# Optimization experiments

Measured on AMD Instinct MI355X. Metric: run time of the kernel, lower is better.

Reference implementation:

```python
import jax, jax.numpy as jnp
import numpy as np

KS = 3          # kernel size
PAD = 1         # padding
N = KS * KS     # number of sampling taps (9)


def setup_inputs() -> dict:
    key = jax.random.key(0)
    k0, k1, k2 = jax.random.split(key, 3)
    B, Cin, Cout, H, W = 4, 64, 64, 128, 128
    x = jax.random.normal(k0, (B, Cin, H, W), jnp.float32)
    # offset conv is zero-initialized in the original; use small random weights
    # so the sampling pattern is actually irregular (post-training behavior)
    w_off = jax.random.normal(k1, (2 * N, Cin, KS, KS), jnp.float32) * 0.05
    b_off = jnp.zeros((2 * N,), jnp.float32)
    w_def = jax.random.normal(k2, (Cout, Cin, KS, KS), jnp.float32) / np.float32(np.sqrt(Cin * N))
    b_def = jnp.zeros((Cout,), jnp.float32)
    return {"x": x, "w_off": w_off, "b_off": b_off, "w_def": w_def, "b_def": b_def}


def _conv3x3(x, w, b):
    y = jax.lax.conv_general_dilated(
        x, w, window_strides=(1, 1), padding=((PAD, PAD), (PAD, PAD)),
        dimension_numbers=("NCHW", "OIHW", "NCHW"))
    return y + b[None, :, None, None]


def _deform_forward(x, w_off, b_off, w_def, b_def):
    B, C, H, W = x.shape
    Cout = w_def.shape[0]
    offset = _conv3x3(x, w_off, b_off)                 # [B, 2N, H, W]

    xp = jnp.pad(x, ((0, 0), (0, 0), (PAD, PAD), (PAD, PAD)))  # zero pad
    Hp, Wp = H + 2 * PAD, W + 2 * PAD

    # sampling positions p = p0 + pn + offset (coords in padded frame)
    r = jnp.arange(-(KS // 2), KS // 2 + 1, dtype=x.dtype)
    pn_x = jnp.repeat(r, KS)          # [-1,-1,-1, 0,0,0, 1,1,1]
    pn_y = jnp.tile(r, KS)            # [-1, 0, 1, ...]
    p0x = jnp.arange(1, H + 1, dtype=x.dtype)[None, :, None, None]  # [1,H,1,1]
    p0y = jnp.arange(1, W + 1, dtype=x.dtype)[None, None, :, None]  # [1,1,W,1]
    offx = offset[:, :N].transpose(0, 2, 3, 1)          # [B,H,W,N]
    offy = offset[:, N:].transpose(0, 2, 3, 1)
    px = p0x + pn_x[None, None, None, :] + offx          # [B,H,W,N]
    py = p0y + pn_y[None, None, None, :] + offy

    # integer corners (floor has zero grad == detach in torch ref)
    flx, fly = jnp.floor(px), jnp.floor(py)
    qlx = jnp.clip(flx, 0, Hp - 1)
    qly = jnp.clip(fly, 0, Wp - 1)
    qrx = jnp.clip(flx + 1, 0, Hp - 1)
    qry = jnp.clip(fly + 1, 0, Wp - 1)
    pxc = jnp.clip(px, 0, Hp - 1)
    pyc = jnp.clip(py, 0, Wp - 1)

    # bilinear weights (matches torch DeformConv2D formulas)
    g_lt = (1 + (qlx - pxc)) * (1 + (qly - pyc))
    g_rb = (1 - (qrx - pxc)) * (1 - (qry - pyc))
    g_lb = (1 + (qlx - pxc)) * (1 - (qry - pyc))
    g_rt = (1 - (qrx - pxc)) * (1 + (qly - pyc))

    xf = xp.reshape(B, C, Hp * Wp)

    def gather(xfb, ix, iy):
        idx = (ix * Wp + iy).astype(jnp.int32).reshape(-1)
        return xfb[:, idx].reshape(C, H, W, N)

    g4 = jax.vmap(gather)
    x_lt = g4(xf, qlx, qly)   # [B,C,H,W,N]
    x_rb = g4(xf, qrx, qry)
    x_lb = g4(xf, qlx, qry)
    x_rt = g4(xf, qrx, qly)

    x_off = (g_lt[:, None] * x_lt + g_rb[:, None] * x_rb
             + g_lb[:, None] * x_lb + g_rt[:, None] * x_rt)  # [B,C,H,W,N]

    out = jnp.einsum("bchwn,ocn->bohw", x_off, w_def.reshape(Cout, C, N))
    return out + b_def[None, :, None, None]


def reference(x, w_off, b_off, w_def, b_def):
    return _deform_forward(x, w_off, b_off, w_def, b_def)
```

## Files before the change

kernel.cpp:

```cpp
#include <hip/hip_runtime.h>

#define B_   4
#define CIN  64
#define COUT 64
#define H_   128
#define W_   128
#define NOFF 18
#define HW   (H_ * W_)
#define HP   130
#define WP   130

typedef __attribute__((ext_vector_type(8))) short bf16x8;
typedef __attribute__((ext_vector_type(4))) float f32x4;

__device__ __forceinline__ unsigned short f2bf(float f) {
    unsigned int u = __float_as_uint(f);
    return (unsigned short)((u + 0x7fffu + ((u >> 16) & 1u)) >> 16);
}

__global__ __launch_bounds__(256) void k_wt(
    const float* __restrict__ w_def, const float* __restrict__ w_off,
    unsigned short* __restrict__ wB, unsigned short* __restrict__ wBo)
{
    const int i = blockIdx.x * 256 + threadIdx.x;
    if (i < 18 * 4 * 64) {
        const int kblk = i >> 8;
        const int nblk = (i >> 6) & 3;
        const int lane = i & 63;
        const int o = nblk * 16 + (lane & 15);
        unsigned int pk[4];
#pragma unroll
        for (int d = 0; d < 4; ++d) {
            unsigned int v = 0;
#pragma unroll
            for (int e = 0; e < 2; ++e) {
                const int K = kblk * 32 + 8 * (lane >> 4) + d * 2 + e;
                const int n = K >> 6, c = K & 63;
                v |= (unsigned int)f2bf(w_def[((size_t)o * 64 + c) * 9 + n]) << (16 * e);
            }
            pk[d] = v;
        }
        *(uint4*)(wB + (size_t)i * 8) = make_uint4(pk[0], pk[1], pk[2], pk[3]);
    }
    const int j = i - 18 * 4 * 64;
    if (j >= 0 && j < 18 * 2 * 64) {
        const int kblk = j >> 7;
        const int nblk = (j >> 6) & 1;
        const int lane = j & 63;
        const int o = nblk * 16 + (lane & 15);
        unsigned int pk[4];
#pragma unroll
        for (int d = 0; d < 4; ++d) {
            unsigned int v = 0;
#pragma unroll
            for (int e = 0; e < 2; ++e) {
                const int K = kblk * 32 + 8 * (lane >> 4) + d * 2 + e;
                const int n = K >> 6, c = K & 63;
                const float wv = (o < NOFF) ? w_off[((size_t)o * 64 + c) * 9 + n] : 0.f;
                v |= (unsigned int)f2bf(wv) << (16 * e);
            }
            pk[d] = v;
        }
        *(uint4*)(wBo + (size_t)j * 8) = make_uint4(pk[0], pk[1], pk[2], pk[3]);
    }
}

__global__ __launch_bounds__(256) void k_prep(
    const float* __restrict__ x, unsigned short* __restrict__ xt,
    unsigned int* __restrict__ xt2)
{
    const int b  = blockIdx.x / HP;
    const int hp = blockIdx.x - b * HP;
    const int c  = threadIdx.x & 63;
    const int wq = threadIdx.x >> 6;
    const float* xr = x + (((size_t)b * CIN + c) * H_ + (hp - 1)) * W_;
    unsigned short* d1 = xt  + (((size_t)b * HP + hp) * WP) * 64 + c;
    unsigned int*   d2 = xt2 + (((size_t)b * HP + hp) * WP) * 64 + c;
    const bool hin = (hp >= 1 && hp <= H_);
    for (int wp = wq; wp < WP; wp += 4) {
        float v1 = 0.f, v2 = 0.f;
        if (hin) {
            if (wp >= 1 && wp <= W_)       v1 = xr[wp - 1];
            if (wp + 1 >= 1 && wp + 1 <= W_) v2 = xr[wp];
        }
        const unsigned int a1 = f2bf(v1), a2 = f2bf(v2);
        d1[(size_t)wp * 64] = (unsigned short)a1;
        d2[(size_t)wp * 64] = a1 | (a2 << 16);
    }
}

__global__ __launch_bounds__(256) void k_mega(
    const unsigned short* __restrict__ xt, const unsigned int* __restrict__ xt2,
    const unsigned short* __restrict__ wBo, const unsigned short* __restrict__ wB,
    const float* __restrict__ b_off, const float* __restrict__ b_def,
    unsigned short* __restrict__ xoff, float* __restrict__ out)
{
    __shared__ float  off_s[NOFF][64];
    __shared__ uint2  geoI[9][64];
    __shared__ float4 geoG[9][64];

    const int tid   = threadIdx.x;
    const int lane  = tid & 63;
    const int wv    = tid >> 6;
    const int row   = lane & 15;
    const int g     = lane >> 4;
    const int pxblk = blockIdx.x;
    const int b     = pxblk >> 8;
    const int h     = (pxblk >> 1) & 127;
    const int w0    = (pxblk & 1) * 64;

    {
        const unsigned short* xtb = xt + (size_t)b * (HP * WP * 64);
        const unsigned short* Bp  = wBo + (size_t)lane * 8;
        f32x4 acc0 = {0.f, 0.f, 0.f, 0.f};
        f32x4 acc1 = {0.f, 0.f, 0.f, 0.f};
#pragma unroll
        for (int kb = 0; kb < 18; ++kb) {
            const int n  = kb >> 1;
            const int hp = h + n / 3;
            const int wp = w0 + wv * 16 + row + (n % 3);
            const int cb = (kb & 1) * 32 + g * 8;
            const bf16x8 a  = *(const bf16x8*)(xtb + ((size_t)hp * WP + wp) * 64 + cb);
            const bf16x8 b0 = *(const bf16x8*)(Bp + (size_t)(kb * 2 + 0) * 512);
            const bf16x8 b1 = *(const bf16x8*)(Bp + (size_t)(kb * 2 + 1) * 512);
            acc0 = __builtin_amdgcn_mfma_f32_16x16x32_bf16(a, b0, acc0, 0, 0, 0);
            acc1 = __builtin_amdgcn_mfma_f32_16x16x32_bf16(a, b1, acc1, 0, 0, 0);
        }
        const int pxb = wv * 16 + 4 * g;
        {
            const float bias = b_off[row];
#pragma unroll
            for (int r = 0; r < 4; ++r) off_s[row][pxb + r] = acc0[r] + bias;
        }
        if (row < 2) {
            const float bias = b_off[16 + row];
#pragma unroll
            for (int r = 0; r < 4; ++r) off_s[16 + row][pxb + r] = acc1[r] + bias;
        }
    }
    __syncthreads();

    for (int it = tid; it < 576; it += 256) {
        const int pxl = it & 63;
        const int n   = it >> 6;
        const int wpix = w0 + pxl;
        const float ox = off_s[n][pxl];
        const float oy = off_s[n + 9][pxl];
        const float px = (float)(h + n / 3) + ox;
        const float py = (float)(wpix + n % 3) + oy;
        const float flx = floorf(px), fly = floorf(py);
        const float qlx = fminf(fmaxf(flx, 0.f), 129.f);
        const float qly = fminf(fmaxf(fly, 0.f), 129.f);
        const float qrx = fminf(fmaxf(flx + 1.f, 0.f), 129.f);
        const float qry = fminf(fmaxf(fly + 1.f, 0.f), 129.f);
        const float pxc = fminf(fmaxf(px, 0.f), 129.f);
        const float pyc = fminf(fmaxf(py, 0.f), 129.f);
        const float gxl = 1.f + (qlx - pxc);
        const float gxr = 1.f - (qrx - pxc);
        const float gyl = 1.f + (qly - pyc);
        const float gyr = 1.f - (qry - pyc);
        const int xl = (int)qlx, yl = (int)qly, xr = (int)qrx, yr = (int)qry;
        float wyl = gyl, wyr = gyr;
        if (yr == yl) { wyl = gyl + gyr; wyr = 0.f; }
        geoI[n][pxl] = make_uint2((unsigned)((xl * WP + yl) * 256),
                                  (unsigned)((xr * WP + yl) * 256));
        geoG[n][pxl] = make_float4(wyl, wyr, gxl, gxr);
    }
    __syncthreads();

    const char* xtb4 = (const char*)(xt2 + (size_t)b * (HP * WP * 64)) + lane * 4;
    unsigned short* xo = xoff + (size_t)(pxblk * 64) * 576;

#pragma unroll 1
    for (int pxi = 0; pxi < 16; ++pxi) {
        const int pxl = wv * 16 + pxi;
#pragma unroll 3
        for (int n = 0; n < 9; ++n) {
            const uint2  gi = geoI[n][pxl];
            const float4 gg = geoG[n][pxl];
            const unsigned int u1 = *(const unsigned int*)(xtb4 + gi.x);
            const unsigned int u2 = *(const unsigned int*)(xtb4 + gi.y);
            const float s0 = __uint_as_float(u1 << 16);
            const float s1 = __uint_as_float(u1 & 0xffff0000u);
            const float t0 = __uint_as_float(u2 << 16);
            const float t1 = __uint_as_float(u2 & 0xffff0000u);
            const float r1 = fmaf(gg.x, s0, gg.y * s1);
            const float r2 = fmaf(gg.x, t0, gg.y * t1);
            const float v  = fmaf(gg.z, r1, gg.w * r2);
            xo[(size_t)pxl * 576 + n * 64 + lane] = f2bf(v);
        }
    }

    __syncthreads();

    const unsigned short* Ap = xoff + (size_t)(pxblk * 64 + wv * 16 + row) * 576 + g * 8;
    const unsigned short* Bp = wB + (size_t)lane * 8;

    f32x4 acc0 = {0.f, 0.f, 0.f, 0.f};
    f32x4 acc1 = {0.f, 0.f, 0.f, 0.f};
    f32x4 acc2 = {0.f, 0.f, 0.f, 0.f};
    f32x4 acc3 = {0.f, 0.f, 0.f, 0.f};

#pragma unroll 3
    for (int kb = 0; kb < 18; ++kb) {
        const bf16x8 a  = *(const bf16x8*)(Ap + kb * 32);
        const bf16x8 b0 = *(const bf16x8*)(Bp + (size_t)(kb * 4 + 0) * 512);
        const bf16x8 b1 = *(const bf16x8*)(Bp + (size_t)(kb * 4 + 1) * 512);
        const bf16x8 b2 = *(const bf16x8*)(Bp + (size_t)(kb * 4 + 2) * 512);
        const bf16x8 b3 = *(const bf16x8*)(Bp + (size_t)(kb * 4 + 3) * 512);
        acc0 = __builtin_amdgcn_mfma_f32_16x16x32_bf16(a, b0, acc0, 0, 0, 0);
        acc1 = __builtin_amdgcn_mfma_f32_16x16x32_bf16(a, b1, acc1, 0, 0, 0);
        acc2 = __builtin_amdgcn_mfma_f32_16x16x32_bf16(a, b2, acc2, 0, 0, 0);
        acc3 = __builtin_amdgcn_mfma_f32_16x16x32_bf16(a, b3, acc3, 0, 0, 0);
    }

    const int p_base = pxblk * 64 + wv * 16 + 4 * g;
#pragma unroll
    for (int i = 0; i < 4; ++i) {
        const int o = i * 16 + row;
        const float bias = b_def[o];
        const f32x4 A = (i == 0) ? acc0 : (i == 1) ? acc1 : (i == 2) ? acc2 : acc3;
#pragma unroll
        for (int r = 0; r < 4; ++r) {
            const int p  = p_base + r;
            const int bb = p >> 14;
            const int hw = p & 16383;
            out[((size_t)(bb * COUT + o)) * HW + hw] = A[r] + bias;
        }
    }
}

extern "C" void kernel_launch(void* const* d_in, const int* in_sizes, int n_in,
                              void* d_out, int out_size, void* d_ws, size_t ws_size,
                              hipStream_t stream)
{
    const float* x     = (const float*)d_in[0];
    const float* w_off = (const float*)d_in[1];
    const float* b_off = (const float*)d_in[2];
    const float* w_def = (const float*)d_in[3];
    const float* b_def = (const float*)d_in[4];
    float* out = (float*)d_out;

    char* ws = (char*)d_ws;
    unsigned short* wB   = (unsigned short*)(ws + 0);
    unsigned short* wBo  = (unsigned short*)(ws + 73728);
    unsigned short* xt   = (unsigned short*)(ws + 110592);
    unsigned int*   xt2  = (unsigned int*)(ws + 8763392);
    unsigned short* xoff = (unsigned short*)(ws + 26068992);

    k_wt<<<(18 * 4 * 64 + 18 * 2 * 64 + 255) / 256, 256, 0, stream>>>(
        w_def, w_off, wB, wBo);
    k_prep<<<B_ * HP, 256, 0, stream>>>(x, xt, xt2);
    k_mega<<<B_ * HW / 64, 256, 0, stream>>>(xt, xt2, wBo, wB, b_off, b_def,
                                             xoff, out);
}
```

Before: 95.03 us.

## Halve pixels per block, swizzle block order, merge weight prep into input prep

Splits the fused deformable-conv kernel into blocks of 32 pixels instead of 64, doubling the grid and remapping block indices so neighbouring blocks are spread across XCDs. Only two waves run the MFMA offset conv and output GEMM, while all four waves share the bilinear gather. The weight-repacking kernel is folded into the input-prep kernel to remove one launch. The trade is more parallelism for the gather-heavy phase against idle waves during the MFMA phases and more repeated weight reads.

```diff
diff --git a/kernel.cpp b/kernel.cpp
--- a/kernel.cpp
+++ b/kernel.cpp
@@ -18,7 +18,9 @@
     return (unsigned short)((u + 0x7fffu + ((u >> 16) & 1u)) >> 16);
 }
 
-__global__ __launch_bounds__(256) void k_wt(
+__global__ __launch_bounds__(256) void k_prep(
+    const float* __restrict__ x, unsigned short* __restrict__ xt,
+    unsigned int* __restrict__ xt2,
     const float* __restrict__ w_def, const float* __restrict__ w_off,
     unsigned short* __restrict__ wB, unsigned short* __restrict__ wBo)
 {
@@ -63,12 +65,7 @@
         }
         *(uint4*)(wBo + (size_t)j * 8) = make_uint4(pk[0], pk[1], pk[2], pk[3]);
     }
-}
-
-__global__ __launch_bounds__(256) void k_prep(
-    const float* __restrict__ x, unsigned short* __restrict__ xt,
-    unsigned int* __restrict__ xt2)
-{
+
     const int b  = blockIdx.x / HP;
     const int hp = blockIdx.x - b * HP;
     const int c  = threadIdx.x & 63;
@@ -80,7 +77,7 @@
     for (int wp = wq; wp < WP; wp += 4) {
         float v1 = 0.f, v2 = 0.f;
         if (hin) {
-            if (wp >= 1 && wp <= W_)       v1 = xr[wp - 1];
+            if (wp >= 1 && wp <= W_)         v1 = xr[wp - 1];
             if (wp + 1 >= 1 && wp + 1 <= W_) v2 = xr[wp];
         }
         const unsigned int a1 = f2bf(v1), a2 = f2bf(v2);
@@ -89,27 +86,27 @@
     }
 }
 
-__global__ __launch_bounds__(256) void k_mega(
+__global__ __launch_bounds__(256) void k_fuse2(
     const unsigned short* __restrict__ xt, const unsigned int* __restrict__ xt2,
     const unsigned short* __restrict__ wBo, const unsigned short* __restrict__ wB,
     const float* __restrict__ b_off, const float* __restrict__ b_def,
     unsigned short* __restrict__ xoff, float* __restrict__ out)
 {
-    __shared__ float  off_s[NOFF][64];
-    __shared__ uint2  geoI[9][64];
-    __shared__ float4 geoG[9][64];
+    __shared__ float  off_s[NOFF][33];
+    __shared__ uint2  geoI[9][32];
+    __shared__ float4 geoG[9][32];
 
     const int tid   = threadIdx.x;
     const int lane  = tid & 63;
     const int wv    = tid >> 6;
-    const int row   = lane & 15;
-    const int g     = lane >> 4;
-    const int pxblk = blockIdx.x;
-    const int b     = pxblk >> 8;
-    const int h     = (pxblk >> 1) & 127;
-    const int w0    = (pxblk & 1) * 64;
-
-    {
+    const int pxblk = ((blockIdx.x & 7) << 8) | (blockIdx.x >> 3);
+    const int b     = pxblk >> 9;
+    const int h     = (pxblk >> 2) & 127;
+    const int w0    = (pxblk & 3) * 32;
+
+    if (wv < 2) {
+        const int row = lane & 15;
+        const int g   = lane >> 4;
         const unsigned short* xtb = xt + (size_t)b * (HP * WP * 64);
         const unsigned short* Bp  = wBo + (size_t)lane * 8;
         f32x4 acc0 = {0.f, 0.f, 0.f, 0.f};
@@ -140,40 +137,40 @@
     }
     __syncthreads();
 
-    for (int it = tid; it < 576; it += 256) {
-        const int pxl = it & 63;
-        const int n   = it >> 6;
-        const int wpix = w0 + pxl;
-        const float ox = off_s[n][pxl];
-        const float oy = off_s[n + 9][pxl];
-        const float px = (float)(h + n / 3) + ox;
-        const float py = (float)(wpix + n % 3) + oy;
-        const float flx = floorf(px), fly = floorf(py);
-        const float qlx = fminf(fmaxf(flx, 0.f), 129.f);
-        const float qly = fminf(fmaxf(fly, 0.f), 129.f);
-        const float qrx = fminf(fmaxf(flx + 1.f, 0.f), 129.f);
-        const float qry = fminf(fmaxf(fly + 1.f, 0.f), 129.f);
-        const float pxc = fminf(fmaxf(px, 0.f), 129.f);
-        const float pyc = fminf(fmaxf(py, 0.f), 129.f);
-        const float gxl = 1.f + (qlx - pxc);
-        const float gxr = 1.f - (qrx - pxc);
-        const float gyl = 1.f + (qly - pyc);
-        const float gyr = 1.f - (qry - pyc);
-        const int xl = (int)qlx, yl = (int)qly, xr = (int)qrx, yr = (int)qry;
-        float wyl = gyl, wyr = gyr;
-        if (yr == yl) { wyl = gyl + gyr; wyr = 0.f; }
-        geoI[n][pxl] = make_uint2((unsigned)((xl * WP + yl) * 256),
-                                  (unsigned)((xr * WP + yl) * 256));
-        geoG[n][pxl] = make_float4(wyl, wyr, gxl, gxr);
+    if (lane < 32) {
+        const int wpix = w0 + lane;
+        for (int n = wv; n < 9; n += 4) {
+            const float ox = off_s[n][lane];
+            const float oy = off_s[n + 9][lane];
+            const float px = (float)(h + n / 3) + ox;
+            const float py = (float)(wpix + n % 3) + oy;
+            const float flx = floorf(px), fly = floorf(py);
+            const float qlx = fminf(fmaxf(flx, 0.f), 129.f);
+            const float qly = fminf(fmaxf(fly, 0.f), 129.f);
+            const float qrx = fminf(fmaxf(flx + 1.f, 0.f), 129.f);
+            const float qry = fminf(fmaxf(fly + 1.f, 0.f), 129.f);
+            const float pxc = fminf(fmaxf(px, 0.f), 129.f);
+            const float pyc = fminf(fmaxf(py, 0.f), 129.f);
+            const float gxl = 1.f + (qlx - pxc);
+            const float gxr = 1.f - (qrx - pxc);
+            const float gyl = 1.f + (qly - pyc);
+            const float gyr = 1.f - (qry - pyc);
+            const int xl = (int)qlx, yl = (int)qly, xr = (int)qrx, yr = (int)qry;
+            float wyl = gyl, wyr = gyr;
+            if (yr == yl) { wyl = gyl + gyr; wyr = 0.f; }
+            geoI[n][lane] = make_uint2((unsigned)((xl * WP + yl) * 256),
+                                       (unsigned)((xr * WP + yl) * 256));
+            geoG[n][lane] = make_float4(wyl, wyr, gxl, gxr);
+        }
     }
     __syncthreads();
 
     const char* xtb4 = (const char*)(xt2 + (size_t)b * (HP * WP * 64)) + lane * 4;
-    unsigned short* xo = xoff + (size_t)(pxblk * 64) * 576;
+    unsigned short* xo = xoff + (size_t)(pxblk * 32) * 576;
 
 #pragma unroll 1
-    for (int pxi = 0; pxi < 16; ++pxi) {
-        const int pxl = wv * 16 + pxi;
+    for (int pxi = 0; pxi < 8; ++pxi) {
+        const int pxl = wv * 8 + pxi;
 #pragma unroll 3
         for (int n = 0; n < 9; ++n) {
             const uint2  gi = geoI[n][pxl];
@@ -192,8 +189,12 @@
     }
 
     __syncthreads();
-
-    const unsigned short* Ap = xoff + (size_t)(pxblk * 64 + wv * 16 + row) * 576 + g * 8;
+    if (wv >= 2) return;
+
+    const int row = lane & 15;
+    const int g   = lane >> 4;
+
+    const unsigned short* Ap = xoff + (size_t)(pxblk * 32 + wv * 16 + row) * 576 + g * 8;
     const unsigned short* Bp = wB + (size_t)lane * 8;
 
     f32x4 acc0 = {0.f, 0.f, 0.f, 0.f};
@@ -214,7 +215,7 @@
         acc3 = __builtin_amdgcn_mfma_f32_16x16x32_bf16(a, b3, acc3, 0, 0, 0);
     }
 
-    const int p_base = pxblk * 64 + wv * 16 + 4 * g;
+    const int p_base = pxblk * 32 + wv * 16 + 4 * g;
 #pragma unroll
     for (int i = 0; i < 4; ++i) {
         const int o = i * 16 + row;
@@ -248,9 +249,7 @@
     unsigned int*   xt2  = (unsigned int*)(ws + 8763392);
     unsigned short* xoff = (unsigned short*)(ws + 26068992);
 
-    k_wt<<<(18 * 4 * 64 + 18 * 2 * 64 + 255) / 256, 256, 0, stream>>>(
-        w_def, w_off, wB, wBo);
-    k_prep<<<B_ * HP, 256, 0, stream>>>(x, xt, xt2);
-    k_mega<<<B_ * HW / 64, 256, 0, stream>>>(xt, xt2, wBo, wB, b_off, b_def,
-                                             xoff, out);
-}
+    k_prep<<<B_ * HP, 256, 0, stream>>>(x, xt, xt2, w_def, w_off, wB, wBo);
+    k_fuse2<<<B_ * HW / 32, 256, 0, stream>>>(xt, xt2, wBo, wB, b_off, b_def,
+                                              xoff, out);
+}
```

Result: faster. 92.74 us (-2.4%).
